# Performance work log

Hardware: AMD Instinct MI355X
Metric: run time of the kernel (lower is better)

Reference implementation:

```python
import jax, jax.numpy as jnp
import numpy as np

SIZE = 4096
N_ITER = 10
TEMP = 0.1


def setup_inputs() -> dict:
    key = jax.random.key(0)
    kx, kw = jax.random.split(key)
    x = jax.random.normal(kx, (4, 2048, SIZE), dtype=jnp.float32)
    weight = jax.random.normal(kw, (SIZE, SIZE), dtype=jnp.float32)
    r_prev = jnp.zeros((SIZE, 1), dtype=jnp.float32)
    c_prev = jnp.zeros((1, SIZE), dtype=jnp.float32)
    return {"x": x, "weight": weight, "r_prev": r_prev, "c_prev": c_prev}


def reference(x, weight, r_prev, c_prev):
    Q = weight / TEMP  # [S, S]

    def body(i, rc):
        r, c = rc
        r = -jax.nn.logsumexp(Q + c, axis=1, keepdims=True)  # [S, 1]
        c = -jax.nn.logsumexp(Q + r, axis=0, keepdims=True)  # [1, S]
        return (r, c)

    r, c = jax.lax.fori_loop(0, N_ITER, body, (r_prev, c_prev))
    P = jnp.exp(Q + r + c)  # doubly-stochastic-ish [S, S]
    # F.linear(x, P) == x @ P.T
    return jnp.einsum('btd,od->bto', x, P)
```

## Files before the change

kernel.cpp:

```cpp
#include <hip/hip_runtime.h>


#define L2E 1.44269504088896340736f

typedef __attribute__((ext_vector_type(8))) short bf16x8;
typedef __attribute__((ext_vector_type(4))) float f32x4;

__device__ __forceinline__ unsigned short f2bf(float x) {
  unsigned u = __float_as_uint(x);
  u += 0x7fffu + ((u >> 16) & 1u);
  return (unsigned short)(u >> 16);
}
__device__ __forceinline__ float bf2f(short x) {
  return __uint_as_float(((unsigned)(unsigned short)x) << 16);
}

__global__ void prep_e(const float* __restrict__ W, unsigned short* __restrict__ E) {
  const int row = blockIdx.x;
  const int t = threadIdx.x;
  const float* wp = W + ((size_t)row << 12);
  float v[16];
  float m = -3.4e38f;
#pragma unroll
  for (int ch = 0; ch < 4; ++ch) {
    float4 wv = *(const float4*)(wp + ch * 1024 + t * 4);
    float a0 = 10.f * wv.x, a1 = 10.f * wv.y, a2 = 10.f * wv.z, a3 = 10.f * wv.w;
    v[ch * 4 + 0] = a0; v[ch * 4 + 1] = a1; v[ch * 4 + 2] = a2; v[ch * 4 + 3] = a3;
    m = fmaxf(m, fmaxf(fmaxf(a0, a1), fmaxf(a2, a3)));
  }
#pragma unroll
  for (int off = 32; off > 0; off >>= 1) m = fmaxf(m, __shfl_xor(m, off));
  __shared__ float sm[4];
  if ((t & 63) == 0) sm[t >> 6] = m;
  __syncthreads();
  m = fmaxf(fmaxf(sm[0], sm[1]), fmaxf(sm[2], sm[3]));
  unsigned short* ep = E + ((size_t)row << 12);
#pragma unroll
  for (int ch = 0; ch < 4; ++ch) {
    ushort4 o;
    o.x = f2bf(exp2f((v[ch * 4 + 0] - m) * L2E));
    o.y = f2bf(exp2f((v[ch * 4 + 1] - m) * L2E));
    o.z = f2bf(exp2f((v[ch * 4 + 2] - m) * L2E));
    o.w = f2bf(exp2f((v[ch * 4 + 3] - m) * L2E));
    *(ushort4*)(ep + ch * 1024 + t * 4) = o;
  }
}

__global__ void transpose_bf(const unsigned short* __restrict__ E,
                             unsigned short* __restrict__ ET) {
  __shared__ unsigned short tile[64][66];
  const int t = threadIdx.x;
  const int r = t >> 3;
  const int c8 = (t & 7) << 3;
  const size_t i0 = (size_t)blockIdx.y << 6;
  const size_t j0 = (size_t)blockIdx.x << 6;
#pragma unroll
  for (int h = 0; h < 2; ++h) {
    bf16x8 vv = *(const bf16x8*)(E + (i0 + h * 32 + r) * 4096 + j0 + c8);
#pragma unroll
    for (int e = 0; e < 8; ++e) tile[h * 32 + r][c8 + e] = (unsigned short)vv[e];
  }
  __syncthreads();
#pragma unroll
  for (int h = 0; h < 2; ++h) {
    bf16x8 vv;
#pragma unroll
    for (int e = 0; e < 8; ++e) vv[e] = (short)tile[c8 + e][h * 32 + r];
    *(bf16x8*)(ET + (j0 + h * 32 + r) * 4096 + i0 + c8) = vv;
  }
}

__global__ void init_u(const float* __restrict__ c_prev, float* __restrict__ u) {
  const int i = blockIdx.x * 256 + threadIdx.x;
  u[i] = exp2f(c_prev[i] * L2E);
}

__global__ void recip_mv(const unsigned short* __restrict__ M,
                         const float* __restrict__ uin, float* __restrict__ vout) {
  const int t = threadIdx.x;
  const int l = t & 63, w = t >> 6;
  const int row = (blockIdx.x << 2) + w;
  const unsigned short* mp = M + ((size_t)row << 12);
  float s = 0.f;
#pragma unroll
  for (int ch = 0; ch < 8; ++ch) {
    const int j = (ch << 9) + (l << 3);
    bf16x8 e = *(const bf16x8*)(mp + j);
    const float4 u0 = *(const float4*)(uin + j);
    const float4 u1 = *(const float4*)(uin + j + 4);
    s = fmaf(bf2f(e[0]), u0.x, s);
    s = fmaf(bf2f(e[1]), u0.y, s);
    s = fmaf(bf2f(e[2]), u0.z, s);
    s = fmaf(bf2f(e[3]), u0.w, s);
    s = fmaf(bf2f(e[4]), u1.x, s);
    s = fmaf(bf2f(e[5]), u1.y, s);
    s = fmaf(bf2f(e[6]), u1.z, s);
    s = fmaf(bf2f(e[7]), u1.w, s);
  }
#pragma unroll
  for (int off = 32; off > 0; off >>= 1) s += __shfl_xor(s, off);
  if (l == 0) vout[row] = 1.f / s;
}

__global__ void scale_x(const float* __restrict__ X, const float* __restrict__ u,
                        unsigned short* __restrict__ Y) {
  const size_t idx = ((size_t)blockIdx.x * 256 + threadIdx.x) * 4;
  const int col = (int)(idx & 4095);
  float4 xv = *(const float4*)(X + idx);
  float4 uu = *(const float4*)(u + col);
  ushort4 o;
  o.x = f2bf(xv.x * uu.x);
  o.y = f2bf(xv.y * uu.y);
  o.z = f2bf(xv.z * uu.z);
  o.w = f2bf(xv.w * uu.w);
  *(ushort4*)(Y + idx) = o;
}

__global__ __launch_bounds__(512, 2) void gemm_bt(const unsigned short* __restrict__ A,
                                                  const unsigned short* __restrict__ B,
                                                  const float* __restrict__ vscale,
                                                  float* __restrict__ C) {
  __shared__ unsigned short lds[65536];
  const int t = threadIdx.x;
  const int l = t & 63;
  const int w = t >> 6;
  const int wm = w >> 2, wn = w & 3;

  int pid = blockIdx.x;
  pid = (pid & 7) * 64 + (pid >> 3);
  const int grp = pid >> 6;
  const int rem = pid & 63;
  const int bm = (grp << 2) + (rem & 3);
  const int bn = rem >> 2;
  const int m0 = bm << 8;
  const int n0 = bn << 8;

  const int ca = (((t & 3) ^ ((t >> 3) & 3)) << 3);
  const unsigned short* gA = A + (size_t)(m0 + (t >> 2)) * 4096 + ca;
  const unsigned short* gB = B + (size_t)(n0 + (t >> 2)) * 4096 + ca;

  const int xc = (((l >> 4) ^ ((l >> 1) & 3)) << 3);
  const int aOff = (wm * 128 + (l & 15)) * 32 + xc;
  const int bOff = (wn * 64 + (l & 15)) * 32 + xc;

  auto stageA = [&](int kt) {
    const int b = kt & 3;
    const unsigned short* g = gA + (size_t)kt * 32;
#pragma unroll
    for (int ra = 0; ra < 2; ++ra)
      __builtin_amdgcn_global_load_lds(
          (const __attribute__((address_space(1))) void*)(g + (size_t)ra * 524288),
          (__attribute__((address_space(3))) void*)((char*)lds + b * 16384 + ra * 8192 + w * 1024),
          16, 0, 0);
  };
  auto stageB = [&](int kt) {
    const int b = kt & 3;
    const unsigned short* g = gB + (size_t)kt * 32;
#pragma unroll
    for (int ra = 0; ra < 2; ++ra)
      __builtin_amdgcn_global_load_lds(
          (const __attribute__((address_space(1))) void*)(g + (size_t)ra * 524288),
          (__attribute__((address_space(3))) void*)((char*)lds + 65536 + b * 16384 + ra * 8192 + w * 1024),
          16, 0, 0);
  };

  f32x4 acc[8][4] = {};

  stageA(0); stageB(0);
  stageA(1); stageB(1);
  stageA(2); stageB(2);
  asm volatile("s_waitcnt vmcnt(8)" ::: "memory");
  __builtin_amdgcn_s_barrier();

  bf16x8 cA[4], cB[4], nA[4], nB[4], hfr[4];
#pragma unroll
  for (int i = 0; i < 4; ++i) cA[i] = *(const bf16x8*)(lds + aOff + i * 512);
#pragma unroll
  for (int j = 0; j < 4; ++j) cB[j] = *(const bf16x8*)(lds + 32768 + bOff + j * 512);

#define PHASE_PAIR(KT, CA, CB, NA, NB)                                            \
  {                                                                               \
    const int kt_ = (KT);                                                         \
    const int buf_ = kt_ & 3;                                                     \
    const unsigned short* aL = lds + buf_ * 8192 + aOff;                          \
    const unsigned short* bL = lds + 32768 + buf_ * 8192 + bOff;                  \
      \
    _Pragma("unroll")                                                             \
    for (int i = 0; i < 4; ++i) hfr[i] = *(const bf16x8*)(aL + (4 + i) * 512);    \
    if (kt_ <= 124) stageA(kt_ + 3);                                              \
    if (kt_ <= 124)      asm volatile("s_waitcnt vmcnt(6)" ::: "memory");         \
    else if (kt_ == 125) asm volatile("s_waitcnt vmcnt(4)" ::: "memory");         \
    else                 asm volatile("s_waitcnt vmcnt(0)" ::: "memory");         \
    __builtin_amdgcn_sched_barrier(0);                                            \
    __builtin_amdgcn_s_barrier();                                                 \
    __builtin_amdgcn_s_setprio(1);                                                \
    _Pragma("unroll")                                                             \
    for (int i = 0; i < 4; ++i)                                                   \
      _Pragma("unroll")                                                           \
      for (int j = 0; j < 4; ++j)                                                 \
        acc[i][j] = __builtin_amdgcn_mfma_f32_16x16x32_bf16(CA[i], CB[j],         \
                                                            acc[i][j], 0, 0, 0); \
    __builtin_amdgcn_s_setprio(0);                                                \
    __builtin_amdgcn_s_barrier();                                                 \
        \
    if (kt_ <= 126) {                                                             \
      const unsigned short* aN = lds + ((kt_ + 1) & 3) * 8192 + aOff;             \
      const unsigned short* bN = lds + 32768 + ((kt_ + 1) & 3) * 8192 + bOff;     \
      _Pragma("unroll")                                                           \
      for (int i = 0; i < 4; ++i) NA[i] = *(const bf16x8*)(aN + i * 512);         \
      _Pragma("unroll")                                                           \
      for (int j = 0; j < 4; ++j) NB[j] = *(const bf16x8*)(bN + j * 512);         \
    }                                                                             \
    if (kt_ <= 124) stageB(kt_ + 3);                                              \
    __builtin_amdgcn_sched_barrier(0);                                            \
    __builtin_amdgcn_s_barrier();                                                 \
    __builtin_amdgcn_s_setprio(1);                                                \
    _Pragma("unroll")                                                             \
    for (int i = 0; i < 4; ++i)                                                   \
      _Pragma("unroll")                                                           \
      for (int j = 0; j < 4; ++j)                                                 \
        acc[4 + i][j] = __builtin_amdgcn_mfma_f32_16x16x32_bf16(hfr[i], CB[j],    \
                                                                acc[4 + i][j],   \
                                                                0, 0, 0);         \
    __builtin_amdgcn_s_setprio(0);                                                \
    __builtin_amdgcn_s_barrier();                                                 \
  }

  for (int kt = 0; kt < 128; kt += 2) {
    PHASE_PAIR(kt, cA, cB, nA, nB)
    PHASE_PAIR(kt + 1, nA, nB, cA, cB)
  }
#undef PHASE_PAIR

  const int crow = (l >> 4) << 2;
  const int ccol = l & 15;
#pragma unroll
  for (int j = 0; j < 4; ++j) {
    const int colj = n0 + (wn << 6) + (j << 4) + ccol;
    const float vs = vscale[colj];
#pragma unroll
    for (int i = 0; i < 8; ++i) {
      const int rowi = m0 + (wm << 7) + (i << 4) + crow;
#pragma unroll
      for (int q = 0; q < 4; ++q)
        C[((size_t)(rowi + q) << 12) + colj] = acc[i][j][q] * vs;
    }
  }
}

extern "C" void kernel_launch(void* const* d_in, const int* in_sizes, int n_in,
                              void* d_out, int out_size, void* d_ws, size_t ws_size,
                              hipStream_t stream) {
  const float* x      = (const float*)d_in[0];
  const float* weight = (const float*)d_in[1];
  const float* c_prev = (const float*)d_in[3];
  float* out = (float*)d_out;

  char* ws = (char*)d_ws;
  float* u = (float*)ws;
  float* v = (float*)(ws + (16 << 10));
  unsigned short* E  = (unsigned short*)(ws + (64 << 10));
  unsigned short* ET = E + (size_t)4096 * 4096;
  unsigned short* xb = ET;

  prep_e<<<4096, 256, 0, stream>>>(weight, E);
  transpose_bf<<<dim3(64, 64), 256, 0, stream>>>(E, ET);
  init_u<<<16, 256, 0, stream>>>(c_prev, u);

  for (int it = 0; it < 10; ++it) {
    recip_mv<<<1024, 256, 0, stream>>>(E, u, v);
    recip_mv<<<1024, 256, 0, stream>>>(ET, v, u);
  }

  scale_x<<<32768, 256, 0, stream>>>(x, u, xb);

  gemm_bt<<<512, 512, 0, stream>>>(xb, E, v, out);
}
```

Measured before the change: 444.9 us.

## Merge GEMM phase halves into single barrier phase and split matvec rows across waves

The GEMM main loop goes from two barrier-separated MFMA halves per k-tile to one phase. That phase loads the next tile's fragments early, issues both A and B global-to-LDS stages together, and uses adjusted vmcnt waits. This aims to halve the barrier count per k-step, at the cost of more live registers and possible LDS read/write hazards on the 4-deep ring buffer. The Sinkhorn matvec also splits each row across two waves combined through shared memory, doubling the grid to 2048 blocks for more parallelism in the latency-bound iterations.

```diff
diff --git a/kernel.cpp b/kernel.cpp
--- a/kernel.cpp
+++ b/kernel.cpp
@@ -79,15 +79,17 @@
                          const float* __restrict__ uin, float* __restrict__ vout) {
   const int t = threadIdx.x;
   const int l = t & 63, w = t >> 6;
-  const int row = (blockIdx.x << 2) + w;
-  const unsigned short* mp = M + ((size_t)row << 12);
+  const int row = (blockIdx.x << 1) + (w >> 1);
+  const int half = (w & 1) << 11;
+  const unsigned short* mp = M + ((size_t)row << 12) + half;
+  const float* up = uin + half;
   float s = 0.f;
 #pragma unroll
-  for (int ch = 0; ch < 8; ++ch) {
+  for (int ch = 0; ch < 4; ++ch) {
     const int j = (ch << 9) + (l << 3);
     bf16x8 e = *(const bf16x8*)(mp + j);
-    const float4 u0 = *(const float4*)(uin + j);
-    const float4 u1 = *(const float4*)(uin + j + 4);
+    const float4 u0 = *(const float4*)(up + j);
+    const float4 u1 = *(const float4*)(up + j + 4);
     s = fmaf(bf2f(e[0]), u0.x, s);
     s = fmaf(bf2f(e[1]), u0.y, s);
     s = fmaf(bf2f(e[2]), u0.z, s);
@@ -99,7 +101,10 @@
   }
 #pragma unroll
   for (int off = 32; off > 0; off >>= 1) s += __shfl_xor(s, off);
-  if (l == 0) vout[row] = 1.f / s;
+  __shared__ float sm[4];
+  if (l == 0) sm[w] = s;
+  __syncthreads();
+  if (t < 2) vout[(blockIdx.x << 1) + t] = 1.f / (sm[t << 1] + sm[(t << 1) + 1]);
 }
 
 __global__ void scale_x(const float* __restrict__ X, const float* __restrict__ u,
@@ -169,28 +174,32 @@
   stageA(0); stageB(0);
   stageA(1); stageB(1);
   stageA(2); stageB(2);
-  asm volatile("s_waitcnt vmcnt(8)" ::: "memory");
+  asm volatile("s_waitcnt vmcnt(4)" ::: "memory");
   __builtin_amdgcn_s_barrier();
 
-  bf16x8 cA[4], cB[4], nA[4], nB[4], hfr[4];
+  bf16x8 cA[4], cB[4], nA[4], nB[4], hiA[4];
 #pragma unroll
   for (int i = 0; i < 4; ++i) cA[i] = *(const bf16x8*)(lds + aOff + i * 512);
 #pragma unroll
   for (int j = 0; j < 4; ++j) cB[j] = *(const bf16x8*)(lds + 32768 + bOff + j * 512);
 
-#define PHASE_PAIR(KT, CA, CB, NA, NB)                                            \
+#define PHASE(KT, CLA, CLB, NLA, NLB)                                             \
   {                                                                               \
     const int kt_ = (KT);                                                         \
-    const int buf_ = kt_ & 3;                                                     \
-    const unsigned short* aL = lds + buf_ * 8192 + aOff;                          \
-    const unsigned short* bL = lds + 32768 + buf_ * 8192 + bOff;                  \
-      \
+    const unsigned short* aL = lds + (kt_ & 3) * 8192 + aOff;                     \
     _Pragma("unroll")                                                             \
-    for (int i = 0; i < 4; ++i) hfr[i] = *(const bf16x8*)(aL + (4 + i) * 512);    \
-    if (kt_ <= 124) stageA(kt_ + 3);                                              \
-    if (kt_ <= 124)      asm volatile("s_waitcnt vmcnt(6)" ::: "memory");         \
-    else if (kt_ == 125) asm volatile("s_waitcnt vmcnt(4)" ::: "memory");         \
-    else                 asm volatile("s_waitcnt vmcnt(0)" ::: "memory");         \
+    for (int i = 0; i < 4; ++i) hiA[i] = *(const bf16x8*)(aL + (4 + i) * 512);    \
+    if (kt_ <= 126) {                                                             \
+      const unsigned short* aN = lds + ((kt_ + 1) & 3) * 8192 + aOff;             \
+      const unsigned short* bN = lds + 32768 + ((kt_ + 1) & 3) * 8192 + bOff;     \
+      _Pragma("unroll")                                                           \
+      for (int i = 0; i < 4; ++i) NLA[i] = *(const bf16x8*)(aN + i * 512);        \
+      _Pragma("unroll")                                                           \
+      for (int j = 0; j < 4; ++j) NLB[j] = *(const bf16x8*)(bN + j * 512);        \
+    }                                                                             \
+    if (kt_ <= 124) { stageA(kt_ + 3); stageB(kt_ + 3); }                         \
+    if (kt_ <= 124)      asm volatile("s_waitcnt vmcnt(4)" ::: "memory");         \
+    else if (kt_ == 125) asm volatile("s_waitcnt vmcnt(0)" ::: "memory");         \
     __builtin_amdgcn_sched_barrier(0);                                            \
     __builtin_amdgcn_s_barrier();                                                 \
     __builtin_amdgcn_s_setprio(1);                                                \
@@ -198,28 +207,13 @@
     for (int i = 0; i < 4; ++i)                                                   \
       _Pragma("unroll")                                                           \
       for (int j = 0; j < 4; ++j)                                                 \
-        acc[i][j] = __builtin_amdgcn_mfma_f32_16x16x32_bf16(CA[i], CB[j],         \
+        acc[i][j] = __builtin_amdgcn_mfma_f32_16x16x32_bf16(CLA[i], CLB[j],       \
                                                             acc[i][j], 0, 0, 0); \
-    __builtin_amdgcn_s_setprio(0);                                                \
-    __builtin_amdgcn_s_barrier();                                                 \
-        \
-    if (kt_ <= 126) {                                                             \
-      const unsigned short* aN = lds + ((kt_ + 1) & 3) * 8192 + aOff;             \
-      const unsigned short* bN = lds + 32768 + ((kt_ + 1) & 3) * 8192 + bOff;     \
-      _Pragma("unroll")                                                           \
-      for (int i = 0; i < 4; ++i) NA[i] = *(const bf16x8*)(aN + i * 512);         \
-      _Pragma("unroll")                                                           \
-      for (int j = 0; j < 4; ++j) NB[j] = *(const bf16x8*)(bN + j * 512);         \
-    }                                                                             \
-    if (kt_ <= 124) stageB(kt_ + 3);                                              \
-    __builtin_amdgcn_sched_barrier(0);                                            \
-    __builtin_amdgcn_s_barrier();                                                 \
-    __builtin_amdgcn_s_setprio(1);                                                \
     _Pragma("unroll")                                                             \
     for (int i = 0; i < 4; ++i)                                                   \
       _Pragma("unroll")                                                           \
       for (int j = 0; j < 4; ++j)                                                 \
-        acc[4 + i][j] = __builtin_amdgcn_mfma_f32_16x16x32_bf16(hfr[i], CB[j],    \
+        acc[4 + i][j] = __builtin_amdgcn_mfma_f32_16x16x32_bf16(hiA[i], CLB[j],   \
                                                                 acc[4 + i][j],   \
                                                                 0, 0, 0);         \
     __builtin_amdgcn_s_setprio(0);                                                \
@@ -227,10 +221,10 @@
   }
 
   for (int kt = 0; kt < 128; kt += 2) {
-    PHASE_PAIR(kt, cA, cB, nA, nB)
-    PHASE_PAIR(kt + 1, nA, nB, cA, cB)
-  }
-#undef PHASE_PAIR
+    PHASE(kt, cA, cB, nA, nB)
+    PHASE(kt + 1, nA, nB, cA, cB)
+  }
+#undef PHASE
 
   const int crow = (l >> 4) << 2;
   const int ccol = l & 15;
@@ -268,8 +262,8 @@
   init_u<<<16, 256, 0, stream>>>(c_prev, u);
 
   for (int it = 0; it < 10; ++it) {
-    recip_mv<<<1024, 256, 0, stream>>>(E, u, v);
-    recip_mv<<<1024, 256, 0, stream>>>(ET, v, u);
+    recip_mv<<<2048, 256, 0, stream>>>(E, u, v);
+    recip_mv<<<2048, 256, 0, stream>>>(ET, v, u);
   }
 
   scale_x<<<32768, 256, 0, stream>>>(x, u, xb);
```

Measured after the change: 450.6 us. Within noise of the previous version (+1.3%).
